# Kernel tuning notes

Measured on AMD Instinct MI355X. Metric: run time of the kernel, lower is better.

The kernel has to match this reference:

```python
import jax, jax.numpy as jnp
import numpy as np

KERNEL = 7
PAD = 3
STRIDE = 1
DIL = 1
HEADS = 8
OUT_CH = 256


def _unfold(x, k, pad, stride, dil):
    # x: (B, C, H, W) -> (B, C*k*k, Ho, Wo); channel ordering (C, kh, kw),
    # matching torch.nn.Unfold's channel-major layout.
    return jax.lax.conv_general_dilated_patches(
        x, filter_shape=(k, k), window_strides=(stride, stride),
        padding=((pad, pad), (pad, pad)), rhs_dilation=(dil, dil))


def _conv1x1(x, w, b):
    # 1x1 conv == per-pixel matmul. w: (O, C), b: (O,)
    return jnp.einsum('bchw,oc->bohw', x, w) + b[None, :, None, None]


def setup_inputs() -> dict:
    key = jax.random.key(0)
    ks = jax.random.split(key, 11)
    B, C, H, W = 2, 256, 64, 64
    f = lambda k, sh: jax.random.normal(k, sh, dtype=jnp.float32)
    ws = 1.0 / np.sqrt(C).astype(np.float32)
    return dict(
        queries=f(ks[0], (B, C, H, W)),
        keys=f(ks[1], (B, C, H, W)),
        values=f(ks[2], (B, C, H, W)),
        wq=f(ks[3], (OUT_CH, C)) * ws, bq=f(ks[4], (OUT_CH,)) * 0.01,
        wk=f(ks[5], (OUT_CH, C)) * ws, bk=f(ks[6], (OUT_CH,)) * 0.01,
        wv=f(ks[7], (OUT_CH, C)) * ws, bv=f(ks[8], (OUT_CH,)) * 0.01,
        wo=f(ks[9], (OUT_CH, OUT_CH)) * ws, bo=f(ks[10], (OUT_CH,)) * 0.01,
    )


def reference(queries, keys, values, wq, bq, wk, bk, wv, bv, wo, bo):
    B = values.shape[0]
    d = OUT_CH // HEADS
    K2 = KERNEL * KERNEL
    q = _conv1x1(queries, wq, bq)
    k = _conv1x1(keys, wk, bk)
    v = _conv1x1(values, wv, bv)
    # query 'unfold' with kernel 1, stride STRIDE == strided subsample
    q = q[:, :, ::STRIDE, ::STRIDE]
    Ho, Wo = q.shape[-2], q.shape[-1]
    L = Ho * Wo
    q = q.reshape(B, HEADS, d, L)                                  # (B,h,d,L)
    kp = _unfold(k, KERNEL, PAD, STRIDE, DIL).reshape(B, HEADS, d, K2, L)
    vp = _unfold(v, KERNEL, PAD, STRIDE, DIL).reshape(B, HEADS, d, K2, L)
    scale = jnp.float32(1.0 / np.sqrt(OUT_CH))                     # note: sqrt(out_channels), per source
    attn = jnp.einsum('bhdl,bhdkl->bhlk', q, kp) * scale           # (B,h,L,K2)
    attn = jax.nn.softmax(attn, axis=-1)
    out = jnp.einsum('bhdkl,bhlk->bhdl', vp, attn)                 # (B,h,d,L)
    out = out.reshape(B, OUT_CH, Ho, Wo)
    return _conv1x1(out, wo, bo)
```

## Files before the change

### kernel.cpp

```cpp
#include <hip/hip_runtime.h>
#include <hip/hip_bf16.h>
#include <math.h>

#define B_ 2
#define C_ 256
#define H_ 64
#define W_ 64
#define L_ 4096
#define HEADS_ 8
#define DH_ 32
#define CG_ 8
#define K_ 7
#define PAD_ 3
#define K2_ 49
#define PW_ 70
#define PPIX_ 4900
#define PADT_ ((size_t)B_*HEADS_*CG_*PPIX_)
#define WS_STR 72

typedef short bf16x8 __attribute__((ext_vector_type(8)));
typedef float f32x4  __attribute__((ext_vector_type(4)));

__device__ inline unsigned short f2bf(float f) {
    union { float f; unsigned u; } uf; uf.f = f;
    unsigned r = uf.u + 0x7fffu + ((uf.u >> 16) & 1u);
    return (unsigned short)(r >> 16);
}
__device__ inline unsigned pk2(float a, float b) {
    return (unsigned)f2bf(a) | ((unsigned)f2bf(b) << 16);
}

__global__ __launch_bounds__(256) void prep(
    const float* __restrict__ wq, const float* __restrict__ wk,
    const float* __restrict__ wv, const float* __restrict__ wo,
    unsigned* __restrict__ wb)
{
    int idx = blockIdx.x*256 + threadIdx.x;
    const float* src = (idx < 32768) ? wq : (idx < 65536) ? wk : (idx < 98304) ? wv : wo;
    int off = (idx & 32767) * 2;
    wb[idx] = pk2(src[off], src[off+1]);
}

__global__ __launch_bounds__(256) void qkv_mfma(
    const float* __restrict__ q_in, const float* __restrict__ k_in, const float* __restrict__ v_in,
    const unsigned* __restrict__ wb,
    const float* __restrict__ bq, const float* __restrict__ bk, const float* __restrict__ bv,
    uint2* __restrict__ qt2, uint2* __restrict__ kt2, uint2* __restrict__ vt2)
{
    const int z = blockIdx.z;
    const int tid = threadIdx.x;

    if (z == 6) {
        const int flat = blockIdx.x + 64*blockIdx.y;
        const uint2 zz = make_uint2(0u, 0u);
        for (size_t idx = (size_t)flat*256 + tid; idx < PADT_; idx += 128*256) {
            int cell = (int)(idx % PPIX_);
            int px = cell % PW_, py = cell / PW_;
            if (px < PAD_ || px >= PW_-PAD_ || py < PAD_ || py >= PW_-PAD_) {
                kt2[idx] = zz;
                vt2[idx] = zz;
            }
        }
        return;
    }

    const int which = z >> 1;
    const int b = z & 1;
    const float* X = (which==0) ? q_in : (which==1 ? k_in : v_in);
    const unsigned* wbp = wb + which*32768;
    const float* bias = (which==0) ? bq : (which==1 ? bk : bv);

    const int y    = blockIdx.x;
    const int l0   = y * 64;
    const int o_t0 = blockIdx.y * 128;
    const int lane = tid & 63, wave = tid >> 6;
    const int orow = lane & 15, kgrp = lane >> 4;

    __shared__ short Ws[128*WS_STR];
    __shared__ short Xs[64*WS_STR];

    f32x4 acc[2][4] = {};

    for (int ch = 0; ch < 4; ++ch) {
        const int c0 = ch*64;
        #pragma unroll
        for (int i = 0; i < 8; ++i) {
            int o  = i*16 + (tid>>4);
            int c4 = tid & 15;
            uint2 v = *reinterpret_cast<const uint2*>(wbp + (size_t)(o_t0 + o)*128 + (c0>>1) + c4*2);
            *reinterpret_cast<uint2*>(&Ws[o*WS_STR + c4*4]) = v;
        }
        #pragma unroll
        for (int i = 0; i < 4; ++i) {
            int c_loc = (tid>>4) + i*16;
            int l4    = (tid&15)*4;
            float4 xv = *reinterpret_cast<const float4*>(&X[(size_t)(b*C_ + c0 + c_loc)*L_ + l0 + l4]);
            Xs[(l4+0)*WS_STR + c_loc] = (short)f2bf(xv.x);
            Xs[(l4+1)*WS_STR + c_loc] = (short)f2bf(xv.y);
            Xs[(l4+2)*WS_STR + c_loc] = (short)f2bf(xv.z);
            Xs[(l4+3)*WS_STR + c_loc] = (short)f2bf(xv.w);
        }
        __syncthreads();
        #pragma unroll
        for (int kk = 0; kk < 2; ++kk) {
            bf16x8 af[2], bfr[4];
            #pragma unroll
            for (int fo = 0; fo < 2; ++fo)
                af[fo] = *reinterpret_cast<const bf16x8*>(&Ws[(wave*32 + fo*16 + orow)*WS_STR + kk*32 + kgrp*8]);
            #pragma unroll
            for (int fn = 0; fn < 4; ++fn)
                bfr[fn] = *reinterpret_cast<const bf16x8*>(&Xs[(fn*16 + orow)*WS_STR + kk*32 + kgrp*8]);
            #pragma unroll
            for (int fo = 0; fo < 2; ++fo)
                #pragma unroll
                for (int fn = 0; fn < 4; ++fn)
                    acc[fo][fn] = __builtin_amdgcn_mfma_f32_16x16x32_bf16(af[fo], bfr[fn], acc[fo][fn], 0, 0, 0);
        }
        __syncthreads();
    }

    #pragma unroll
    for (int fo = 0; fo < 2; ++fo) {
        const int og = o_t0 + wave*32 + fo*16 + kgrp*4;
        const float4 b4 = *reinterpret_cast<const float4*>(&bias[og]);
        const size_t p = (size_t)(b*64 + (og >> 2));
        #pragma unroll
        for (int fn = 0; fn < 4; ++fn) {
            const int xl = fn*16 + orow;
            uint2 r = make_uint2(pk2(acc[fo][fn][0] + b4.x, acc[fo][fn][1] + b4.y),
                                 pk2(acc[fo][fn][2] + b4.z, acc[fo][fn][3] + b4.w));
            if (which == 0) {
                qt2[p*L_ + l0 + xl] = r;
            } else {
                uint2* dst = (which==1) ? kt2 : vt2;
                dst[p*PPIX_ + (size_t)(y+PAD_)*PW_ + (xl+PAD_)] = r;
            }
        }
    }
}

__global__ __launch_bounds__(256) void local_attn(
    uint2* __restrict__ qt2, const uint2* __restrict__ kt2, const uint2* __restrict__ vt2)
{
    const int tid = threadIdx.x;
    const int w = tid >> 6, x = tid & 63;
    const int bid = blockIdx.x;
    const int plane = bid & 15;
    const int y = bid >> 4;

    const uint2* kb = kt2 + (size_t)plane*CG_*PPIX_;
    const uint2* vb = vt2 + (size_t)plane*CG_*PPIX_;
    uint2* qpl = qt2 + (size_t)plane*CG_*L_;

    __shared__ float S[K2_][64];

    const float scale = 0.0625f;

    float lg[2][K_] = {};
    #pragma unroll
    for (int cg=0; cg<CG_; ++cg) {
        uint2 qu = qpl[(size_t)cg*L_ + y*W_ + x];
        const float qx = __uint_as_float(qu.x << 16);
        const float qy = __uint_as_float(qu.x & 0xffff0000u);
        const float qz = __uint_as_float(qu.y << 16);
        const float qw = __uint_as_float(qu.y & 0xffff0000u);
        #pragma unroll
        for (int rr=0; rr<2; ++rr) {
            const int r = w + rr*4;
            if (r > 6) continue;
            const uint2* row = kb + (size_t)cg*PPIX_ + (size_t)(y + r)*PW_ + x;
            #pragma unroll
            for (int kx=0; kx<K_; ++kx) {
                uint2 kk = row[kx];
                float k0 = __uint_as_float(kk.x << 16);
                float k1 = __uint_as_float(kk.x & 0xffff0000u);
                float k2 = __uint_as_float(kk.y << 16);
                float k3 = __uint_as_float(kk.y & 0xffff0000u);
                lg[rr][kx] = fmaf(qx,k0, fmaf(qy,k1, fmaf(qz,k2, fmaf(qw,k3, lg[rr][kx]))));
            }
        }
    }
    #pragma unroll
    for (int rr=0; rr<2; ++rr) {
        const int r = w + rr*4;
        if (r <= 6) {
            #pragma unroll
            for (int kx=0; kx<K_; ++kx) S[r*K_+kx][x] = __expf(lg[rr][kx]*scale);
        }
    }
    __syncthreads();

    float sum = 0.f;
    #pragma unroll
    for (int i=0;i<K2_;++i) sum += S[i][x];
    const float inv = 1.0f/sum;

    const int cg0 = w*2, cg1 = w*2 + 1;
    float4 a0 = make_float4(0.f,0.f,0.f,0.f);
    float4 a1 = make_float4(0.f,0.f,0.f,0.f);
    #pragma unroll
    for (int r=0; r<K_; ++r) {
        const uint2* row0 = vb + (size_t)cg0*PPIX_ + (size_t)(y + r)*PW_ + x;
        const uint2* row1 = vb + (size_t)cg1*PPIX_ + (size_t)(y + r)*PW_ + x;
        #pragma unroll
        for (int kx=0; kx<K_; ++kx) {
            const float p = S[r*K_+kx][x];
            uint2 u0 = row0[kx];
            uint2 u1 = row1[kx];
            a0.x = fmaf(p, __uint_as_float(u0.x << 16),        a0.x);
            a0.y = fmaf(p, __uint_as_float(u0.x & 0xffff0000u), a0.y);
            a0.z = fmaf(p, __uint_as_float(u0.y << 16),        a0.z);
            a0.w = fmaf(p, __uint_as_float(u0.y & 0xffff0000u), a0.w);
            a1.x = fmaf(p, __uint_as_float(u1.x << 16),        a1.x);
            a1.y = fmaf(p, __uint_as_float(u1.x & 0xffff0000u), a1.y);
            a1.z = fmaf(p, __uint_as_float(u1.y << 16),        a1.z);
            a1.w = fmaf(p, __uint_as_float(u1.y & 0xffff0000u), a1.w);
        }
    }
    qpl[(size_t)cg0*L_ + y*W_ + x] = make_uint2(pk2(a0.x*inv, a0.y*inv), pk2(a0.z*inv, a0.w*inv));
    qpl[(size_t)cg1*L_ + y*W_ + x] = make_uint2(pk2(a1.x*inv, a1.y*inv), pk2(a1.z*inv, a1.w*inv));
}

__global__ __launch_bounds__(256) void out_mfma(
    const uint2* __restrict__ qt2, const unsigned* __restrict__ wb,
    const float* __restrict__ bo, float* __restrict__ out)
{
    const int b    = blockIdx.z;
    const int l0   = blockIdx.x * 64;
    const int o_t0 = blockIdx.y * 64;
    const unsigned* wbp = wb + 3*32768;
    const int tid  = threadIdx.x;
    const int lane = tid & 63, wave = tid >> 6;
    const int orow = lane & 15, kgrp = lane >> 4;

    __shared__ short Ws[64*WS_STR];
    __shared__ short Xs[64*WS_STR];

    f32x4 acc[4] = {};
    const int cq  = tid >> 6;
    const int lst = tid & 63;

    for (int ch = 0; ch < 4; ++ch) {
        const int c0 = ch*64;
        #pragma unroll
        for (int i = 0; i < 4; ++i) {
            int o  = i*16 + (tid>>4);
            int c4 = tid & 15;
            uint2 v = *reinterpret_cast<const uint2*>(wbp + (size_t)(o_t0 + o)*128 + (c0>>1) + c4*2);
            *reinterpret_cast<uint2*>(&Ws[o*WS_STR + c4*4]) = v;
        }
        #pragma unroll
        for (int i = 0; i < 4; ++i) {
            int c4i = i*4 + cq;
            uint2 v = qt2[(size_t)(b*64 + (c0>>2) + c4i)*L_ + l0 + lst];
            *reinterpret_cast<uint2*>(&Xs[lst*WS_STR + c4i*4]) = v;
        }
        __syncthreads();
        #pragma unroll
        for (int kk = 0; kk < 2; ++kk) {
            bf16x8 af, bfr[4];
            af = *reinterpret_cast<const bf16x8*>(&Ws[(wave*16 + orow)*WS_STR + kk*32 + kgrp*8]);
            #pragma unroll
            for (int fn = 0; fn < 4; ++fn)
                bfr[fn] = *reinterpret_cast<const bf16x8*>(&Xs[(fn*16 + orow)*WS_STR + kk*32 + kgrp*8]);
            #pragma unroll
            for (int fn = 0; fn < 4; ++fn)
                acc[fn] = __builtin_amdgcn_mfma_f32_16x16x32_bf16(af, bfr[fn], acc[fn], 0, 0, 0);
        }
        __syncthreads();
    }

    {
        const int o_base = o_t0 + wave*16 + kgrp*4;
        #pragma unroll
        for (int fn = 0; fn < 4; ++fn) {
            const int xl = fn*16 + orow;
            #pragma unroll
            for (int r = 0; r < 4; ++r)
                out[(size_t)(b*C_ + o_base + r)*L_ + l0 + xl] = acc[fn][r] + bo[o_base + r];
        }
    }
}

extern "C" void kernel_launch(void* const* d_in, const int* in_sizes, int n_in,
                              void* d_out, int out_size, void* d_ws, size_t ws_size,
                              hipStream_t stream) {
    const float* queries = (const float*)d_in[0];
    const float* keys    = (const float*)d_in[1];
    const float* values  = (const float*)d_in[2];
    const float* wq = (const float*)d_in[3];
    const float* bq = (const float*)d_in[4];
    const float* wk = (const float*)d_in[5];
    const float* bk = (const float*)d_in[6];
    const float* wv = (const float*)d_in[7];
    const float* bv = (const float*)d_in[8];
    const float* wo = (const float*)d_in[9];
    const float* bo = (const float*)d_in[10];
    float* out = (float*)d_out;

    uint2* qt2 = (uint2*)d_ws;
    uint2* kt2 = qt2 + (size_t)B_*HEADS_*CG_*L_;
    uint2* vt2 = kt2 + PADT_;
    unsigned* wb = (unsigned*)(vt2 + PADT_);

    prep<<<512, 256, 0, stream>>>(wq, wk, wv, wo, wb);
    qkv_mfma<<<dim3(64, 2, 7), 256, 0, stream>>>(queries, keys, values, wb, bq, bk, bv, qt2, kt2, vt2);
    local_attn<<<1024, 256, 0, stream>>>(qt2, kt2, vt2);
    out_mfma<<<dim3(64, 4, 2), 256, 0, stream>>>(qt2, wb, bo, out);
}
```

Measured before the change: 53.26 us.

## Switch intermediates from bf16 to fp16 with packed dot and half2 FMA

Converts all intermediate storage and the MFMA GEMMs from bf16 to fp16, using hardware packed round-toward-zero conversion instead of software rounding. In the attention kernel the QK logits use fdot2 on packed halves, and the PV accumulation runs in packed half2 per kernel row before being added into fp32. This is meant to cut ALU work for unpacking, converting and FMAs in the local attention and conversion paths. It risks fp16 overflow or accuracy loss, since the pre-conv inputs are unnormalized and partial sums are kept in half precision.

```diff
diff --git a/kernel.cpp b/kernel.cpp
--- a/kernel.cpp
+++ b/kernel.cpp
@@ -1,5 +1,5 @@
 #include <hip/hip_runtime.h>
-#include <hip/hip_bf16.h>
+#include <hip/hip_fp16.h>
 #include <math.h>
 
 #define B_ 2
@@ -18,16 +18,17 @@
 #define PADT_ ((size_t)B_*HEADS_*CG_*PPIX_)
 #define WS_STR 72
 
-typedef short bf16x8 __attribute__((ext_vector_type(8)));
-typedef float f32x4  __attribute__((ext_vector_type(4)));
-
-__device__ inline unsigned short f2bf(float f) {
-    union { float f; unsigned u; } uf; uf.f = f;
-    unsigned r = uf.u + 0x7fffu + ((uf.u >> 16) & 1u);
-    return (unsigned short)(r >> 16);
-}
-__device__ inline unsigned pk2(float a, float b) {
-    return (unsigned)f2bf(a) | ((unsigned)f2bf(b) << 16);
+typedef _Float16 f16x8 __attribute__((ext_vector_type(8)));
+typedef _Float16 h2    __attribute__((ext_vector_type(2)));
+typedef float    f32x4 __attribute__((ext_vector_type(4)));
+
+__device__ inline h2 u2h(unsigned u) { union { unsigned u; h2 h; } c; c.u = u; return c.h; }
+__device__ inline h2 cvt2h(float a, float b) {
+    auto r = __builtin_amdgcn_cvt_pkrtz(a, b);
+    union { decltype(r) s; h2 d; } c; c.s = r; return c.d;
+}
+__device__ inline unsigned pkh(float a, float b) {
+    union { h2 h; unsigned u; } c; c.h = cvt2h(a, b); return c.u;
 }
 
 __global__ __launch_bounds__(256) void prep(
@@ -38,7 +39,7 @@
     int idx = blockIdx.x*256 + threadIdx.x;
     const float* src = (idx < 32768) ? wq : (idx < 65536) ? wk : (idx < 98304) ? wv : wo;
     int off = (idx & 32767) * 2;
-    wb[idx] = pk2(src[off], src[off+1]);
+    wb[idx] = pkh(src[off], src[off+1]);
 }
 
 __global__ __launch_bounds__(256) void qkv_mfma(
@@ -76,8 +77,8 @@
     const int lane = tid & 63, wave = tid >> 6;
     const int orow = lane & 15, kgrp = lane >> 4;
 
-    __shared__ short Ws[128*WS_STR];
-    __shared__ short Xs[64*WS_STR];
+    __shared__ _Float16 Ws[128*WS_STR];
+    __shared__ _Float16 Xs[64*WS_STR];
 
     f32x4 acc[2][4] = {};
 
@@ -95,26 +96,26 @@
             int c_loc = (tid>>4) + i*16;
             int l4    = (tid&15)*4;
             float4 xv = *reinterpret_cast<const float4*>(&X[(size_t)(b*C_ + c0 + c_loc)*L_ + l0 + l4]);
-            Xs[(l4+0)*WS_STR + c_loc] = (short)f2bf(xv.x);
-            Xs[(l4+1)*WS_STR + c_loc] = (short)f2bf(xv.y);
-            Xs[(l4+2)*WS_STR + c_loc] = (short)f2bf(xv.z);
-            Xs[(l4+3)*WS_STR + c_loc] = (short)f2bf(xv.w);
+            Xs[(l4+0)*WS_STR + c_loc] = (_Float16)xv.x;
+            Xs[(l4+1)*WS_STR + c_loc] = (_Float16)xv.y;
+            Xs[(l4+2)*WS_STR + c_loc] = (_Float16)xv.z;
+            Xs[(l4+3)*WS_STR + c_loc] = (_Float16)xv.w;
         }
         __syncthreads();
         #pragma unroll
         for (int kk = 0; kk < 2; ++kk) {
-            bf16x8 af[2], bfr[4];
+            f16x8 af[2], bfr[4];
             #pragma unroll
             for (int fo = 0; fo < 2; ++fo)
-                af[fo] = *reinterpret_cast<const bf16x8*>(&Ws[(wave*32 + fo*16 + orow)*WS_STR + kk*32 + kgrp*8]);
+                af[fo] = *reinterpret_cast<const f16x8*>(&Ws[(wave*32 + fo*16 + orow)*WS_STR + kk*32 + kgrp*8]);
             #pragma unroll
             for (int fn = 0; fn < 4; ++fn)
-                bfr[fn] = *reinterpret_cast<const bf16x8*>(&Xs[(fn*16 + orow)*WS_STR + kk*32 + kgrp*8]);
+                bfr[fn] = *reinterpret_cast<const f16x8*>(&Xs[(fn*16 + orow)*WS_STR + kk*32 + kgrp*8]);
             #pragma unroll
             for (int fo = 0; fo < 2; ++fo)
                 #pragma unroll
                 for (int fn = 0; fn < 4; ++fn)
-                    acc[fo][fn] = __builtin_amdgcn_mfma_f32_16x16x32_bf16(af[fo], bfr[fn], acc[fo][fn], 0, 0, 0);
+                    acc[fo][fn] = __builtin_amdgcn_mfma_f32_16x16x32_f16(af[fo], bfr[fn], acc[fo][fn], 0, 0, 0);
         }
         __syncthreads();
     }
@@ -127,8 +128,8 @@
         #pragma unroll
         for (int fn = 0; fn < 4; ++fn) {
             const int xl = fn*16 + orow;
-            uint2 r = make_uint2(pk2(acc[fo][fn][0] + b4.x, acc[fo][fn][1] + b4.y),
-                                 pk2(acc[fo][fn][2] + b4.z, acc[fo][fn][3] + b4.w));
+            uint2 r = make_uint2(pkh(acc[fo][fn][0] + b4.x, acc[fo][fn][1] + b4.y),
+                                 pkh(acc[fo][fn][2] + b4.z, acc[fo][fn][3] + b4.w));
             if (which == 0) {
                 qt2[p*L_ + l0 + xl] = r;
             } else {
@@ -160,10 +161,7 @@
     #pragma unroll
     for (int cg=0; cg<CG_; ++cg) {
         uint2 qu = qpl[(size_t)cg*L_ + y*W_ + x];
-        const float qx = __uint_as_float(qu.x << 16);
-        const float qy = __uint_as_float(qu.x & 0xffff0000u);
-        const float qz = __uint_as_float(qu.y << 16);
-        const float qw = __uint_as_float(qu.y & 0xffff0000u);
+        const h2 q01 = u2h(qu.x), q23 = u2h(qu.y);
         #pragma unroll
         for (int rr=0; rr<2; ++rr) {
             const int r = w + rr*4;
@@ -172,11 +170,8 @@
             #pragma unroll
             for (int kx=0; kx<K_; ++kx) {
                 uint2 kk = row[kx];
-                float k0 = __uint_as_float(kk.x << 16);
-                float k1 = __uint_as_float(kk.x & 0xffff0000u);
-                float k2 = __uint_as_float(kk.y << 16);
-                float k3 = __uint_as_float(kk.y & 0xffff0000u);
-                lg[rr][kx] = fmaf(qx,k0, fmaf(qy,k1, fmaf(qz,k2, fmaf(qw,k3, lg[rr][kx]))));
+                lg[rr][kx] = __builtin_amdgcn_fdot2(q01, u2h(kk.x), lg[rr][kx], false);
+                lg[rr][kx] = __builtin_amdgcn_fdot2(q23, u2h(kk.y), lg[rr][kx], false);
             }
         }
     }
@@ -202,23 +197,25 @@
     for (int r=0; r<K_; ++r) {
         const uint2* row0 = vb + (size_t)cg0*PPIX_ + (size_t)(y + r)*PW_ + x;
         const uint2* row1 = vb + (size_t)cg1*PPIX_ + (size_t)(y + r)*PW_ + x;
+        h2 ra0 = (h2)0, ra1 = (h2)0, rb0 = (h2)0, rb1 = (h2)0;
         #pragma unroll
         for (int kx=0; kx<K_; ++kx) {
             const float p = S[r*K_+kx][x];
+            const h2 p2 = cvt2h(p, p);
             uint2 u0 = row0[kx];
             uint2 u1 = row1[kx];
-            a0.x = fmaf(p, __uint_as_float(u0.x << 16),        a0.x);
-            a0.y = fmaf(p, __uint_as_float(u0.x & 0xffff0000u), a0.y);
-            a0.z = fmaf(p, __uint_as_float(u0.y << 16),        a0.z);
-            a0.w = fmaf(p, __uint_as_float(u0.y & 0xffff0000u), a0.w);
-            a1.x = fmaf(p, __uint_as_float(u1.x << 16),        a1.x);
-            a1.y = fmaf(p, __uint_as_float(u1.x & 0xffff0000u), a1.y);
-            a1.z = fmaf(p, __uint_as_float(u1.y << 16),        a1.z);
-            a1.w = fmaf(p, __uint_as_float(u1.y & 0xffff0000u), a1.w);
-        }
-    }
-    qpl[(size_t)cg0*L_ + y*W_ + x] = make_uint2(pk2(a0.x*inv, a0.y*inv), pk2(a0.z*inv, a0.w*inv));
-    qpl[(size_t)cg1*L_ + y*W_ + x] = make_uint2(pk2(a1.x*inv, a1.y*inv), pk2(a1.z*inv, a1.w*inv));
+            ra0 += p2 * u2h(u0.x);
+            ra1 += p2 * u2h(u0.y);
+            rb0 += p2 * u2h(u1.x);
+            rb1 += p2 * u2h(u1.y);
+        }
+        a0.x += (float)ra0[0]; a0.y += (float)ra0[1];
+        a0.z += (float)ra1[0]; a0.w += (float)ra1[1];
+        a1.x += (float)rb0[0]; a1.y += (float)rb0[1];
+        a1.z += (float)rb1[0]; a1.w += (float)rb1[1];
+    }
+    qpl[(size_t)cg0*L_ + y*W_ + x] = make_uint2(pkh(a0.x*inv, a0.y*inv), pkh(a0.z*inv, a0.w*inv));
+    qpl[(size_t)cg1*L_ + y*W_ + x] = make_uint2(pkh(a1.x*inv, a1.y*inv), pkh(a1.z*inv, a1.w*inv));
 }
 
 __global__ __launch_bounds__(256) void out_mfma(
@@ -233,8 +230,8 @@
     const int lane = tid & 63, wave = tid >> 6;
     const int orow = lane & 15, kgrp = lane >> 4;
 
-    __shared__ short Ws[64*WS_STR];
-    __shared__ short Xs[64*WS_STR];
+    __shared__ _Float16 Ws[64*WS_STR];
+    __shared__ _Float16 Xs[64*WS_STR];
 
     f32x4 acc[4] = {};
     const int cq  = tid >> 6;
@@ -258,14 +255,14 @@
         __syncthreads();
         #pragma unroll
         for (int kk = 0; kk < 2; ++kk) {
-            bf16x8 af, bfr[4];
-            af = *reinterpret_cast<const bf16x8*>(&Ws[(wave*16 + orow)*WS_STR + kk*32 + kgrp*8]);
+            f16x8 af, bfr[4];
+            af = *reinterpret_cast<const f16x8*>(&Ws[(wave*16 + orow)*WS_STR + kk*32 + kgrp*8]);
             #pragma unroll
             for (int fn = 0; fn < 4; ++fn)
-                bfr[fn] = *reinterpret_cast<const bf16x8*>(&Xs[(fn*16 + orow)*WS_STR + kk*32 + kgrp*8]);
+                bfr[fn] = *reinterpret_cast<const f16x8*>(&Xs[(fn*16 + orow)*WS_STR + kk*32 + kgrp*8]);
             #pragma unroll
             for (int fn = 0; fn < 4; ++fn)
-                acc[fn] = __builtin_amdgcn_mfma_f32_16x16x32_bf16(af, bfr[fn], acc[fn], 0, 0, 0);
+                acc[fn] = __builtin_amdgcn_mfma_f32_16x16x32_f16(af, bfr[fn], acc[fn], 0, 0, 0);
         }
         __syncthreads();
     }
```

Result: faster. 52.05 us (-2.3%).
